# Performance work log

Measured on AMD Instinct MI355X. Metric: run time of the kernel, lower is better.

The kernel has to match this reference:

```python
import jax, jax.numpy as jnp
import numpy as np

B, T, H, NH = 2, 2048, 2048, 16
HD = H // NH
EPS = 1e-5

def gelu_tanh(x):
    c = jnp.sqrt(jnp.asarray(2.0 / jnp.pi, x.dtype))
    return 0.5 * x * (1.0 + jnp.tanh(c * (x + 0.044715 * x * x * x)))

def layer_norm(x, scale, shift):
    mean = jnp.mean(x, axis=-1, keepdims=True)
    var = jnp.mean((x - mean) ** 2, axis=-1, keepdims=True)  # unbiased=False
    return scale * ((x - mean) / jnp.sqrt(var + EPS)) + shift

def setup_inputs() -> dict:
    key = jax.random.key(0)
    ks = jax.random.split(key, 8)
    s = 0.02
    return {
        "x": jax.random.normal(ks[0], (B, T, H), dtype=jnp.float32),
        "wq": jax.random.normal(ks[1], (H, H), dtype=jnp.float32) * s,
        "wk": jax.random.normal(ks[2], (H, H), dtype=jnp.float32) * s,
        "wv": jax.random.normal(ks[3], (H, H), dtype=jnp.float32) * s,
        "wo": jax.random.normal(ks[4], (H, H), dtype=jnp.float32) * s,
        "ln1_scale": jnp.ones((H,), jnp.float32),
        "ln1_shift": jnp.zeros((H,), jnp.float32),
        "ln2_scale": jnp.ones((H,), jnp.float32),
        "ln2_shift": jnp.zeros((H,), jnp.float32),
        "w1": jax.random.normal(ks[5], (H, 4 * H), dtype=jnp.float32) * s,
        "b1": jnp.zeros((4 * H,), jnp.float32),
        "w2": jax.random.normal(ks[6], (4 * H, H), dtype=jnp.float32) * s,
        "b2": jnp.zeros((H,), jnp.float32),
    }

def reference(x, wq, wk, wv, wo, ln1_scale, ln1_shift, ln2_scale, ln2_shift, w1, b1, w2, b2):
    b, t, c = x.shape
    # --- attention sublayer (pre-norm, residual) ---
    h = layer_norm(x, ln1_scale, ln1_shift)
    q = (h @ wq).reshape(b, t, NH, HD).transpose(0, 2, 1, 3)  # [b,nh,t,hd]
    k = (h @ wk).reshape(b, t, NH, HD).transpose(0, 2, 1, 3)
    v = (h @ wv).reshape(b, t, NH, HD).transpose(0, 2, 1, 3)
    scores = jnp.einsum('bhqd,bhkd->bhqk', q, k) / jnp.sqrt(jnp.asarray(HD, jnp.float32))
    causal = jnp.triu(jnp.ones((t, t), jnp.bool_), k=1)
    scores = jnp.where(causal, -jnp.inf, scores)
    weights = jax.nn.softmax(scores, axis=-1)
    attn = jnp.einsum('bhqk,bhkd->bhqd', weights, v)
    attn = attn.transpose(0, 2, 1, 3).reshape(b, t, c)
    x = x + attn @ wo  # dropout is identity (drop_rate=0)
    # --- FFN sublayer ---
    h = layer_norm(x, ln2_scale, ln2_shift)
    h = gelu_tanh(h @ w1 + b1) @ w2 + b2
    return x + h
```

## Files before the change

### kernel.cpp

```cpp
#include <hip/hip_runtime.h>
#include <math.h>

#define HDIM 2048
#define NTOK 4096
#define NHEAD 16
#define HEADD 128
#define TSEQ 2048
#define NBATCH 2

typedef float f32x4 __attribute__((ext_vector_type(4)));
typedef short bf16x8 __attribute__((ext_vector_type(8)));

__device__ __forceinline__ unsigned short f2bf(float f) {
  union { float f; unsigned u; } v; v.f = f;
  unsigned r = v.u + 0x7FFFu + ((v.u >> 16) & 1u);
  return (unsigned short)(r >> 16);
}

__device__ __forceinline__ float gelu_tanh_f(float x) {
  float z = 0.7978845608028654f * (x + 0.044715f * x * x * x);
  float e = __expf(2.f * z);
  float th = 1.f - 2.f / (e + 1.f);
  return 0.5f * x * (1.f + th);
}

#define GLL16(g, l) __builtin_amdgcn_global_load_lds( \
    (const __attribute__((address_space(1))) unsigned int*)(g), \
    (__attribute__((address_space(3))) unsigned int*)(l), 16, 0, 0)

__global__ __launch_bounds__(256) void ln_kernel(const float* __restrict__ in,
                                                 const float* __restrict__ scale,
                                                 const float* __restrict__ shift,
                                                 unsigned short* __restrict__ out) {
  int row = blockIdx.x;
  int t = threadIdx.x;
  const float4* r4 = (const float4*)(in + (size_t)row * HDIM);
  float4 v0 = r4[t];
  float4 v1 = r4[t + 256];
  float sum = v0.x + v0.y + v0.z + v0.w + v1.x + v1.y + v1.z + v1.w;
  float sq  = v0.x*v0.x + v0.y*v0.y + v0.z*v0.z + v0.w*v0.w +
              v1.x*v1.x + v1.y*v1.y + v1.z*v1.z + v1.w*v1.w;
  for (int o = 32; o > 0; o >>= 1) {
    sum += __shfl_down(sum, o);
    sq  += __shfl_down(sq, o);
  }
  __shared__ float red[8];
  __shared__ float stat[2];
  int lane = t & 63, w = t >> 6;
  if (lane == 0) { red[w] = sum; red[4 + w] = sq; }
  __syncthreads();
  if (t == 0) {
    float s = red[0] + red[1] + red[2] + red[3];
    float q = red[4] + red[5] + red[6] + red[7];
    float mean = s / HDIM;
    float var = q / HDIM - mean * mean;
    stat[0] = mean;
    stat[1] = rsqrtf(var + 1e-5f);
  }
  __syncthreads();
  float mean = stat[0], rstd = stat[1];
  const float4* sc4 = (const float4*)scale;
  const float4* sh4 = (const float4*)shift;
  float4 s0 = sc4[t], s1 = sc4[t + 256];
  float4 h0 = sh4[t], h1 = sh4[t + 256];
  ushort4 a, b;
  a.x = f2bf(s0.x * ((v0.x - mean) * rstd) + h0.x);
  a.y = f2bf(s0.y * ((v0.y - mean) * rstd) + h0.y);
  a.z = f2bf(s0.z * ((v0.z - mean) * rstd) + h0.z);
  a.w = f2bf(s0.w * ((v0.w - mean) * rstd) + h0.w);
  b.x = f2bf(s1.x * ((v1.x - mean) * rstd) + h1.x);
  b.y = f2bf(s1.y * ((v1.y - mean) * rstd) + h1.y);
  b.z = f2bf(s1.z * ((v1.z - mean) * rstd) + h1.z);
  b.w = f2bf(s1.w * ((v1.w - mean) * rstd) + h1.w);
  *(ushort4*)&out[(size_t)row * HDIM + t * 4] = a;
  *(ushort4*)&out[(size_t)row * HDIM + 1024 + t * 4] = b;
}

__global__ __launch_bounds__(256) void castT_kernel(const float* __restrict__ W,
                                                    unsigned short* __restrict__ Wt,
                                                    int K, int N) {
  __shared__ float T[64][65];
  int k0 = blockIdx.x * 64, n0 = blockIdx.y * 64;
  int c = threadIdx.x & 15, r = threadIdx.x >> 4;
#pragma unroll
  for (int p = 0; p < 4; p++) {
    int kr = r + p * 16;
    float4 v = *(const float4*)&W[(size_t)(k0 + kr) * N + n0 + c * 4];
    T[kr][c * 4 + 0] = v.x; T[kr][c * 4 + 1] = v.y;
    T[kr][c * 4 + 2] = v.z; T[kr][c * 4 + 3] = v.w;
  }
  __syncthreads();
#pragma unroll
  for (int p = 0; p < 4; p++) {
    int nr = r + p * 16;
    ushort4 o;
    o.x = f2bf(T[c * 4 + 0][nr]);
    o.y = f2bf(T[c * 4 + 1][nr]);
    o.z = f2bf(T[c * 4 + 2][nr]);
    o.w = f2bf(T[c * 4 + 3][nr]);
    *(ushort4*)&Wt[(size_t)(n0 + nr) * K + k0 + c * 4] = o;
  }
}

__global__ __launch_bounds__(256) void gemm_bt(const unsigned short* __restrict__ A,
                                               const unsigned short* __restrict__ Bt,
                                               float* __restrict__ Cf,
                                               unsigned short* __restrict__ Cb,
                                               const float* __restrict__ bias,
                                               const float* __restrict__ resid,
                                               int M, int N, int K, int act_gelu,
                                               int qkv_mode,
                                               unsigned short* __restrict__ Qo,
                                               unsigned short* __restrict__ Ko,
                                               unsigned short* __restrict__ Vto,
                                               int rm, int rn, int xc) {
  __shared__ unsigned short ldsA[128 * 32];
  __shared__ unsigned short ldsB[128 * 32];
  int tid = threadIdx.x;
  int w = tid >> 6, lane = tid & 63;
  int lm = lane & 15, q = lane >> 4;
  int wm = w & 1, wn = w >> 1;

  int flat = blockIdx.y * gridDim.x + blockIdx.x;
  int xcd = flat & 7, l = flat >> 3;
  int tn_l = l % rn, tm_l = l / rn;
  int tm = (xcd / xc) * rm + tm_l;
  int tn = (xcd % xc) * rn + tn_l;
  int m0 = tm * 128, n0 = tn * 128;

  int row0, row1, kbg0, kbg1;
  {
    int o = w * 2048 + lane * 16;
    row0 = o >> 6; kbg0 = ((o >> 4) & 3) ^ ((row0 >> 1) & 3);
    o += 1024;
    row1 = o >> 6; kbg1 = ((o >> 4) & 3) ^ ((row1 >> 1) & 3);
  }
  const unsigned short* pa0 = A  + (size_t)(m0 + row0) * K + kbg0 * 8;
  const unsigned short* pa1 = A  + (size_t)(m0 + row1) * K + kbg1 * 8;
  const unsigned short* pb0 = Bt + (size_t)(n0 + row0) * K + kbg0 * 8;
  const unsigned short* pb1 = Bt + (size_t)(n0 + row1) * K + kbg1 * 8;
  unsigned short* la0 = ldsA + w * 1024;
  unsigned short* la1 = ldsA + w * 1024 + 512;
  unsigned short* lb0 = ldsB + w * 1024;
  unsigned short* lb1 = ldsB + w * 1024 + 512;

  f32x4 acc[4][4] = {};
  int s = (lm >> 1) & 3;
  int aoff[4], boff[4];
#pragma unroll
  for (int t = 0; t < 4; t++) {
    aoff[t] = ((wm * 64 + t * 16 + lm) << 5) + ((q ^ s) << 3);
    boff[t] = ((wn * 64 + t * 16 + lm) << 5) + ((q ^ s) << 3);
  }

  for (int k0 = 0; k0 < K; k0 += 32) {
    GLL16(pa0 + k0, la0);
    GLL16(pa1 + k0, la1);
    GLL16(pb0 + k0, lb0);
    GLL16(pb1 + k0, lb1);
    __syncthreads();
    bf16x8 af[4], bfv[4];
#pragma unroll
    for (int t = 0; t < 4; t++) af[t] = *(const bf16x8*)(ldsA + aoff[t]);
#pragma unroll
    for (int t = 0; t < 4; t++) bfv[t] = *(const bf16x8*)(ldsB + boff[t]);
#pragma unroll
    for (int mi = 0; mi < 4; mi++)
#pragma unroll
      for (int ni = 0; ni < 4; ni++)
        acc[mi][ni] = __builtin_amdgcn_mfma_f32_16x16x32_bf16(af[mi], bfv[ni], acc[mi][ni], 0, 0, 0);
    __syncthreads();
  }

  if (qkv_mode) {
#pragma unroll
    for (int ni = 0; ni < 4; ni++) {
      int n = n0 + wn * 64 + ni * 16 + lm;
      int region = n >> 11;
      int h = (n & 2047) >> 7, d = n & 127;
#pragma unroll
      for (int mi = 0; mi < 4; mi++) {
        int mb = m0 + wm * 64 + mi * 16 + q * 4;
        int b = mb >> 11, t0 = mb & 2047;
        if (region == 2) {
          ushort4 u;
          u.x = f2bf(acc[mi][ni][0]); u.y = f2bf(acc[mi][ni][1]);
          u.z = f2bf(acc[mi][ni][2]); u.w = f2bf(acc[mi][ni][3]);
          *(ushort4*)&Vto[(((size_t)(b * NHEAD + h)) * HEADD + d) * TSEQ + t0] = u;
        } else {
          unsigned short* dst = (region == 0) ? Qo : Ko;
          size_t base2 = (((size_t)(b * NHEAD + h)) * TSEQ + t0) * HEADD + d;
#pragma unroll
          for (int r = 0; r < 4; r++)
            dst[base2 + (size_t)r * HEADD] = f2bf(acc[mi][ni][r]);
        }
      }
    }
    return;
  }

#pragma unroll
  for (int ni = 0; ni < 4; ni++) {
    int n = n0 + wn * 64 + ni * 16 + lm;
    float bv = bias ? bias[n] : 0.f;
#pragma unroll
    for (int mi = 0; mi < 4; mi++) {
#pragma unroll
      for (int r = 0; r < 4; r++) {
        int m = m0 + wm * 64 + mi * 16 + q * 4 + r;
        float v = acc[mi][ni][r] + bv;
        if (act_gelu) v = gelu_tanh_f(v);
        if (resid) v += resid[(size_t)m * N + n];
        if (Cb) Cb[(size_t)m * N + n] = f2bf(v);
        else Cf[(size_t)m * N + n] = v;
      }
    }
  }
}

__global__ __launch_bounds__(256, 4) void attn_mfma(const unsigned short* __restrict__ Qb,
                                                    const unsigned short* __restrict__ Kb,
                                                    const unsigned short* __restrict__ Vtb,
                                                    unsigned short* __restrict__ O) {
  __shared__ unsigned short ldsK[64 * 128];
  __shared__ unsigned short ldsV[128 * 64];
  __shared__ unsigned short ldsP[64 * 64];

  int tid = threadIdx.x;
  int w = tid >> 6, lane = tid & 63;
  int lm = lane & 15, qd = lane >> 4;
  int qt = blockIdx.x, hh = blockIdx.y, bb = blockIdx.z;
  int q0 = qt * 64;
  size_t hbase = (size_t)(bb * NHEAD + hh) * (size_t)(TSEQ * HEADD);
  const unsigned short* Qh = Qb + hbase;
  const unsigned short* Kh = Kb + hbase;
  const unsigned short* Vh = Vtb + hbase;

  bf16x8 qf[4];
  {
    const unsigned short* qp = Qh + (size_t)(q0 + w * 16 + lm) * HEADD + qd * 8;
#pragma unroll
    for (int kc = 0; kc < 4; kc++) qf[kc] = *(const bf16x8*)(qp + kc * 32);
  }

  int koff[4], voff[4], ldst[4];
#pragma unroll
  for (int it = 0; it < 4; it++) {
    int ci = it * 256 + w * 64 + lane;
    int key = ci >> 4, pos = ci & 15;
    koff[it] = key * HEADD + ((pos ^ (key & 15)) << 3);
    int d = ci >> 3, pv = ci & 7;
    voff[it] = d * TSEQ + ((pv ^ (d & 7)) << 3);
    ldst[it] = (it * 256 + w * 64) * 8;
  }

  f32x4 oacc[8] = {};
  float mrow[4], lrow[4];
#pragma unroll
  for (int r = 0; r < 4; r++) { mrow[r] = -3.0e38f; lrow[r] = 0.f; }
  const float scl = 0.08838834764831845f;

  for (int kt = 0; kt <= qt; kt++) {
    int k0 = kt * 64;
    __syncthreads();
#pragma unroll
    for (int it = 0; it < 4; it++) {
      GLL16(Kh + (size_t)k0 * HEADD + koff[it], ldsK + ldst[it]);
      GLL16(Vh + k0 + voff[it], ldsV + ldst[it]);
    }
    __syncthreads();

    f32x4 sacc[4] = {};
#pragma unroll
    for (int kb = 0; kb < 4; kb++) {
#pragma unroll
      for (int kc = 0; kc < 4; kc++) {
        bf16x8 kf = *(const bf16x8*)(ldsK + (kb * 16 + lm) * HEADD + (((kc * 4 + qd) ^ lm) << 3));
        sacc[kb] = __builtin_amdgcn_mfma_f32_16x16x32_bf16(qf[kc], kf, sacc[kb], 0, 0, 0);
      }
    }

    float sv[4][4];
    int qrow_g = q0 + w * 16 + qd * 4;
    bool diag = (kt == qt);
#pragma unroll
    for (int kb = 0; kb < 4; kb++) {
      int key_g = k0 + kb * 16 + lm;
#pragma unroll
      for (int r = 0; r < 4; r++) {
        float x = sacc[kb][r] * scl;
        sv[kb][r] = (diag && key_g > qrow_g + r) ? -3.0e38f : x;
      }
    }
    float mloc[4];
#pragma unroll
    for (int r = 0; r < 4; r++)
      mloc[r] = fmaxf(fmaxf(sv[0][r], sv[1][r]), fmaxf(sv[2][r], sv[3][r]));
#pragma unroll
    for (int dm = 1; dm < 16; dm <<= 1)
#pragma unroll
      for (int r = 0; r < 4; r++) mloc[r] = fmaxf(mloc[r], __shfl_xor(mloc[r], dm));
    float al[4], lloc[4];
#pragma unroll
    for (int r = 0; r < 4; r++) {
      float mnew = fmaxf(mrow[r], mloc[r]);
      al[r] = __expf(mrow[r] - mnew);
      mrow[r] = mnew;
      lloc[r] = 0.f;
    }
#pragma unroll
    for (int kb = 0; kb < 4; kb++) {
#pragma unroll
      for (int r = 0; r < 4; r++) {
        float p = __expf(sv[kb][r] - mrow[r]);
        lloc[r] += p;
        int row = w * 16 + qd * 4 + r;
        int chunk = (kb * 2 + (lm >> 3)) ^ (row & 7);
        ldsP[row * 64 + chunk * 8 + (lm & 7)] = f2bf(p);
      }
    }
#pragma unroll
    for (int dm = 1; dm < 16; dm <<= 1)
#pragma unroll
      for (int r = 0; r < 4; r++) lloc[r] += __shfl_xor(lloc[r], dm);
#pragma unroll
    for (int r = 0; r < 4; r++) lrow[r] = lrow[r] * al[r] + lloc[r];
#pragma unroll
    for (int dt = 0; dt < 8; dt++)
#pragma unroll
      for (int r = 0; r < 4; r++) oacc[dt][r] *= al[r];

    bf16x8 pf[2];
#pragma unroll
    for (int kc2 = 0; kc2 < 2; kc2++)
      pf[kc2] = *(const bf16x8*)(ldsP + (w * 16 + lm) * 64 + (((kc2 * 4 + qd) ^ (lm & 7)) << 3));
#pragma unroll
    for (int dt = 0; dt < 8; dt++) {
#pragma unroll
      for (int kc2 = 0; kc2 < 2; kc2++) {
        bf16x8 vf = *(const bf16x8*)(ldsV + (dt * 16 + lm) * 64 + (((kc2 * 4 + qd) ^ (lm & 7)) << 3));
        oacc[dt] = __builtin_amdgcn_mfma_f32_16x16x32_bf16(pf[kc2], vf, oacc[dt], 0, 0, 0);
      }
    }
  }

  float inv[4];
#pragma unroll
  for (int r = 0; r < 4; r++) inv[r] = 1.f / lrow[r];
#pragma unroll
  for (int dt = 0; dt < 8; dt++) {
#pragma unroll
    for (int r = 0; r < 4; r++) {
      int t = q0 + w * 16 + qd * 4 + r;
      size_t idx = ((size_t)(bb * TSEQ + t)) * HDIM + hh * HEADD + dt * 16 + lm;
      O[idx] = f2bf(oacc[dt][r] * inv[r]);
    }
  }
}

extern "C" void kernel_launch(void* const* d_in, const int* in_sizes, int n_in,
                              void* d_out, int out_size, void* d_ws, size_t ws_size,
                              hipStream_t stream) {
  const float* x         = (const float*)d_in[0];
  const float* wq        = (const float*)d_in[1];
  const float* wk        = (const float*)d_in[2];
  const float* wv        = (const float*)d_in[3];
  const float* wo        = (const float*)d_in[4];
  const float* ln1_scale = (const float*)d_in[5];
  const float* ln1_shift = (const float*)d_in[6];
  const float* ln2_scale = (const float*)d_in[7];
  const float* ln2_shift = (const float*)d_in[8];
  const float* w1        = (const float*)d_in[9];
  const float* b1        = (const float*)d_in[10];
  const float* w2        = (const float*)d_in[11];
  const float* b2        = (const float*)d_in[12];

  char* ws = (char*)d_ws;
  const size_t MB = 1ull << 20;
  unsigned short* h1    = (unsigned short*)(ws);
  float*          x2    = (float*)(ws);
  unsigned short* Qb    = (unsigned short*)(ws + 32 * MB);
  unsigned short* Kb    = (unsigned short*)(ws + 48 * MB);
  unsigned short* Vtb   = (unsigned short*)(ws + 64 * MB);
  unsigned short* attnO = (unsigned short*)(ws + 80 * MB);
  unsigned short* woT   = (unsigned short*)(ws + 96 * MB);
  unsigned short* qkvT  = (unsigned short*)(ws + 104 * MB);
  unsigned short* a1    = (unsigned short*)(ws + 32 * MB);
  unsigned short* h2    = (unsigned short*)(ws + 96 * MB);
  unsigned short* w1T   = (unsigned short*)(ws + 128 * MB);
  unsigned short* w2T   = (unsigned short*)(ws + 160 * MB);

  dim3 blk(256);
  ln_kernel<<<NTOK, blk, 0, stream>>>(x, ln1_scale, ln1_shift, h1);
  castT_kernel<<<dim3(32, 32), blk, 0, stream>>>(wq, qkvT, 2048, 2048);
  castT_kernel<<<dim3(32, 32), blk, 0, stream>>>(wk, qkvT + (size_t)2048 * 2048, 2048, 2048);
  castT_kernel<<<dim3(32, 32), blk, 0, stream>>>(wv, qkvT + (size_t)4096 * 2048, 2048, 2048);
  castT_kernel<<<dim3(32, 32), blk, 0, stream>>>(wo, woT, 2048, 2048);
  castT_kernel<<<dim3(32, 128), blk, 0, stream>>>(w1, w1T, 2048, 8192);
  castT_kernel<<<dim3(128, 32), blk, 0, stream>>>(w2, w2T, 8192, 2048);
  gemm_bt<<<dim3(6144 / 128, 4096 / 128), blk, 0, stream>>>(
      h1, qkvT, nullptr, nullptr, nullptr, nullptr, 4096, 6144, 2048, 0, 1, Qb, Kb, Vtb,
      16, 12, 4);
  attn_mfma<<<dim3(TSEQ / 64, NHEAD, NBATCH), blk, 0, stream>>>(Qb, Kb, Vtb, attnO);
  gemm_bt<<<dim3(2048 / 128, 4096 / 128), blk, 0, stream>>>(
      attnO, woT, x2, nullptr, nullptr, x, 4096, 2048, 2048, 0, 0, nullptr, nullptr, nullptr,
      8, 8, 2);
  ln_kernel<<<NTOK, blk, 0, stream>>>(x2, ln2_scale, ln2_shift, h2);
  gemm_bt<<<dim3(8192 / 128, 4096 / 128), blk, 0, stream>>>(
      h2, w1T, nullptr, a1, b1, nullptr, 4096, 8192, 2048, 1, 0, nullptr, nullptr, nullptr,
      16, 16, 4);
  gemm_bt<<<dim3(2048 / 128, 4096 / 128), blk, 0, stream>>>(
      a1, w2T, (float*)d_out, nullptr, b2, x2, 4096, 2048, 8192, 0, 0, nullptr, nullptr, nullptr,
      8, 8, 2);
}
```

Measured before the change: 1.065 ms.

## Replace 128x128 GEMM with double-buffered 256-row, 8-wave pipelined MFMA GEMM

Replaces the simple single-buffered 128x128 bf16 GEMM with a templated 256xBN tile kernel using 512 threads, K-steps of 64, double-buffered LDS and a hand-scheduled sequence of four phases. Each phase interleaves global-to-LDS staging, LDS fragment loads and MFMA work, with explicit waitcnt, barriers and s_setprio. The goal is to overlap memory latency with compute and raise arithmetic intensity per tile, instead of stalling on a sync after every 32-wide K slice. The cost is larger LDS use and heavy register pressure from the 8xNIT accumulators. The fragile manual vmcnt and barrier choreography also adds correctness risk.

```diff
diff --git a/kernel.cpp b/kernel.cpp
--- a/kernel.cpp
+++ b/kernel.cpp
@@ -102,94 +102,194 @@
   }
 }
 
-__global__ __launch_bounds__(256) void gemm_bt(const unsigned short* __restrict__ A,
-                                               const unsigned short* __restrict__ Bt,
-                                               float* __restrict__ Cf,
-                                               unsigned short* __restrict__ Cb,
-                                               const float* __restrict__ bias,
-                                               const float* __restrict__ resid,
-                                               int M, int N, int K, int act_gelu,
-                                               int qkv_mode,
-                                               unsigned short* __restrict__ Qo,
-                                               unsigned short* __restrict__ Ko,
-                                               unsigned short* __restrict__ Vto,
-                                               int rm, int rn, int xc) {
-  __shared__ unsigned short ldsA[128 * 32];
-  __shared__ unsigned short ldsB[128 * 32];
-  int tid = threadIdx.x;
-  int w = tid >> 6, lane = tid & 63;
-  int lm = lane & 15, q = lane >> 4;
-  int wm = w & 1, wn = w >> 1;
+template<int BN>
+__global__ __launch_bounds__(512, 2) void gemm256(const unsigned short* __restrict__ A,
+                                                  const unsigned short* __restrict__ Bt,
+                                                  float* __restrict__ Cf,
+                                                  unsigned short* __restrict__ Cb,
+                                                  const float* __restrict__ bias,
+                                                  const float* __restrict__ resid,
+                                                  int M, int N, int K, int act_gelu,
+                                                  int qkv_mode,
+                                                  unsigned short* __restrict__ Qo,
+                                                  unsigned short* __restrict__ Ko,
+                                                  unsigned short* __restrict__ Vto,
+                                                  int rm, int rn, int xc) {
+  constexpr int NIT = BN / 64;
+  constexpr int NB  = NIT / 2;
+  constexpr int BSZ = BN * 64;
+
+  __shared__ unsigned short ldsA[2 * 16384];
+  __shared__ unsigned short ldsB[2 * BSZ];
+
+  const int tid = threadIdx.x;
+  const int w = tid >> 6, lane = tid & 63;
+  const int lm = lane & 15, qd = lane >> 4;
+  const int wm = w >> 2, wn = w & 3;
+  const int l8 = lane >> 3, l7 = lane & 7;
 
   int flat = blockIdx.y * gridDim.x + blockIdx.x;
   int xcd = flat & 7, l = flat >> 3;
   int tn_l = l % rn, tm_l = l / rn;
   int tm = (xcd / xc) * rm + tm_l;
   int tn = (xcd % xc) * rn + tn_l;
-  int m0 = tm * 128, n0 = tn * 128;
-
-  int row0, row1, kbg0, kbg1;
-  {
-    int o = w * 2048 + lane * 16;
-    row0 = o >> 6; kbg0 = ((o >> 4) & 3) ^ ((row0 >> 1) & 3);
-    o += 1024;
-    row1 = o >> 6; kbg1 = ((o >> 4) & 3) ^ ((row1 >> 1) & 3);
-  }
-  const unsigned short* pa0 = A  + (size_t)(m0 + row0) * K + kbg0 * 8;
-  const unsigned short* pa1 = A  + (size_t)(m0 + row1) * K + kbg1 * 8;
-  const unsigned short* pb0 = Bt + (size_t)(n0 + row0) * K + kbg0 * 8;
-  const unsigned short* pb1 = Bt + (size_t)(n0 + row1) * K + kbg1 * 8;
-  unsigned short* la0 = ldsA + w * 1024;
-  unsigned short* la1 = ldsA + w * 1024 + 512;
-  unsigned short* lb0 = ldsB + w * 1024;
-  unsigned short* lb1 = ldsB + w * 1024 + 512;
-
-  f32x4 acc[4][4] = {};
-  int s = (lm >> 1) & 3;
-  int aoff[4], boff[4];
-#pragma unroll
-  for (int t = 0; t < 4; t++) {
-    aoff[t] = ((wm * 64 + t * 16 + lm) << 5) + ((q ^ s) << 3);
-    boff[t] = ((wn * 64 + t * 16 + lm) << 5) + ((q ^ s) << 3);
-  }
-
-  for (int k0 = 0; k0 < K; k0 += 32) {
-    GLL16(pa0 + k0, la0);
-    GLL16(pa1 + k0, la1);
-    GLL16(pb0 + k0, lb0);
-    GLL16(pb1 + k0, lb1);
-    __syncthreads();
-    bf16x8 af[4], bfv[4];
-#pragma unroll
-    for (int t = 0; t < 4; t++) af[t] = *(const bf16x8*)(ldsA + aoff[t]);
-#pragma unroll
-    for (int t = 0; t < 4; t++) bfv[t] = *(const bf16x8*)(ldsB + boff[t]);
-#pragma unroll
-    for (int mi = 0; mi < 4; mi++)
-#pragma unroll
-      for (int ni = 0; ni < 4; ni++)
-        acc[mi][ni] = __builtin_amdgcn_mfma_f32_16x16x32_bf16(af[mi], bfv[ni], acc[mi][ni], 0, 0, 0);
-    __syncthreads();
-  }
+  int m0 = tm * 256, n0 = tn * BN;
+
+  const int swz = ((l7 ^ (l8 & 7)) << 3);
+  const int arb = wm * 128 + (w & 3) * 16;
+  const unsigned short* pAs = A + (size_t)(m0 + arb + l8) * K + swz;
+  unsigned short* lAs = ldsA + arb * 64;
+  const int brb = (BN == 256) ? ((w >> 1) * 64 + (w & 1) * 16)
+                              : ((w >> 1) * 32 + (w & 1) * 8);
+  const unsigned short* pBs = Bt + (size_t)(n0 + brb + l8) * K + swz;
+  unsigned short* lBs = ldsB + brb * 64;
+
+  const int ca0 = ((qd ^ l7) << 3);
+  const unsigned short* pAr = ldsA + (wm * 128 + lm) * 64;
+  const unsigned short* pBr = ldsB + (wn * (BN / 4) + lm) * 64;
+
+  f32x4 acc[8][NIT] = {};
+  bf16x8 a[2][4], b[2][NB];
+
+#define STAGE_A(buf, qm, kt) do { \
+    const unsigned short* _s = pAs + (size_t)(qm) * 64 * K + (size_t)(kt) * 64; \
+    unsigned short* _d = lAs + (buf) * 16384 + (qm) * 4096; \
+    GLL16(_s, _d); \
+    GLL16(_s + (size_t)8 * K, _d + 512); \
+  } while (0)
+
+#define STAGE_B(buf, qn, kt) do { \
+    if (BN == 256) { \
+      const unsigned short* _s = pBs + (size_t)(qn) * 32 * K + (size_t)(kt) * 64; \
+      unsigned short* _d = lBs + (buf) * BSZ + (qn) * 2048; \
+      GLL16(_s, _d); \
+      GLL16(_s + (size_t)8 * K, _d + 512); \
+    } else { \
+      const unsigned short* _s = pBs + (size_t)(qn) * 16 * K + (size_t)(kt) * 64; \
+      unsigned short* _d = lBs + (buf) * BSZ + (qn) * 1024; \
+      GLL16(_s, _d); \
+    } \
+  } while (0)
+
+#define LDA(buf, qm) do { \
+    _Pragma("unroll") \
+    for (int mi = 0; mi < 4; mi++) { \
+      a[0][mi] = *(const bf16x8*)(pAr + (buf) * 16384 + (qm) * 4096 + mi * 1024 + ca0); \
+      a[1][mi] = *(const bf16x8*)(pAr + (buf) * 16384 + (qm) * 4096 + mi * 1024 + (ca0 ^ 32)); \
+    } \
+  } while (0)
+
+#define LDB(buf, qn) do { \
+    _Pragma("unroll") \
+    for (int ni = 0; ni < NB; ni++) { \
+      b[0][ni] = *(const bf16x8*)(pBr + (buf) * BSZ + (qn) * (NB * 1024) + ni * 1024 + ca0); \
+      b[1][ni] = *(const bf16x8*)(pBr + (buf) * BSZ + (qn) * (NB * 1024) + ni * 1024 + (ca0 ^ 32)); \
+    } \
+  } while (0)
+
+#define MFMA_PH(qm, qn) do { \
+    __builtin_amdgcn_s_setprio(1); \
+    _Pragma("unroll") \
+    for (int ks = 0; ks < 2; ks++) \
+      _Pragma("unroll") \
+      for (int mi = 0; mi < 4; mi++) \
+        _Pragma("unroll") \
+        for (int ni = 0; ni < NB; ni++) \
+          acc[(qm) * 4 + mi][(qn) * NB + ni] = __builtin_amdgcn_mfma_f32_16x16x32_bf16( \
+              a[ks][mi], b[ks][ni], acc[(qm) * 4 + mi][(qn) * NB + ni], 0, 0, 0); \
+    __builtin_amdgcn_s_setprio(0); \
+  } while (0)
+
+#define BARX() do { asm volatile("" ::: "memory"); __builtin_amdgcn_s_barrier(); \
+                    asm volatile("" ::: "memory"); } while (0)
+#define LGKM0() do { asm volatile("s_waitcnt lgkmcnt(0)" ::: "memory"); \
+                     __builtin_amdgcn_sched_barrier(0); } while (0)
+#define VM_SS() do { if (BN == 256) asm volatile("s_waitcnt vmcnt(6)" ::: "memory"); \
+                     else           asm volatile("s_waitcnt vmcnt(5)" ::: "memory"); } while (0)
+#define VM_0()  do { asm volatile("s_waitcnt vmcnt(0)" ::: "memory"); } while (0)
+
+  const int niter = K >> 7;
+
+  STAGE_A(0, 0, 0); STAGE_B(0, 1, 0); STAGE_A(0, 1, 0); STAGE_B(0, 0, 0);
+  STAGE_A(1, 0, 1); STAGE_B(1, 1, 1); STAGE_A(1, 1, 1);
+  VM_SS();
+  BARX();
+
+  for (int i = 0; i < niter; ++i) {
+    const bool pf = (i + 1 < niter);
+    const int te = 2 * i + 2, to = 2 * i + 3;
+    LDA(0, 0); LDB(0, 0);
+    STAGE_B(1, 0, 2 * i + 1);
+    BARX(); LGKM0();
+    MFMA_PH(0, 0);
+    BARX();
+    LDB(0, 1);
+    if (pf) STAGE_A(0, 0, te);
+    BARX(); LGKM0();
+    MFMA_PH(0, 1);
+    BARX();
+    LDA(0, 1);
+    if (pf) STAGE_B(0, 1, te);
+    BARX(); LGKM0();
+    MFMA_PH(1, 1);
+    BARX();
+    LDB(0, 0);
+    if (pf) STAGE_A(0, 1, te);
+    BARX(); LGKM0();
+    MFMA_PH(1, 0);
+    if (pf) VM_SS(); else VM_0();
+    BARX();
+    LDA(1, 0); LDB(1, 0);
+    if (pf) STAGE_B(0, 0, te);
+    BARX(); LGKM0();
+    MFMA_PH(0, 0);
+    BARX();
+    LDB(1, 1);
+    if (pf) STAGE_A(1, 0, to);
+    BARX(); LGKM0();
+    MFMA_PH(0, 1);
+    BARX();
+    LDA(1, 1);
+    if (pf) STAGE_B(1, 1, to);
+    BARX(); LGKM0();
+    MFMA_PH(1, 1);
+    BARX();
+    LDB(1, 0);
+    if (pf) STAGE_A(1, 1, to);
+    BARX(); LGKM0();
+    MFMA_PH(1, 0);
+    if (pf) VM_SS();
+    BARX();
+  }
+
+#undef STAGE_A
+#undef STAGE_B
+#undef LDA
+#undef LDB
+#undef MFMA_PH
+#undef BARX
+#undef LGKM0
+#undef VM_SS
+#undef VM_0
 
   if (qkv_mode) {
 #pragma unroll
-    for (int ni = 0; ni < 4; ni++) {
-      int n = n0 + wn * 64 + ni * 16 + lm;
+    for (int ni = 0; ni < NIT; ni++) {
+      int n = n0 + wn * (BN / 4) + ni * 16 + lm;
       int region = n >> 11;
       int h = (n & 2047) >> 7, d = n & 127;
 #pragma unroll
-      for (int mi = 0; mi < 4; mi++) {
-        int mb = m0 + wm * 64 + mi * 16 + q * 4;
-        int b = mb >> 11, t0 = mb & 2047;
+      for (int mi = 0; mi < 8; mi++) {
+        int mb = m0 + wm * 128 + mi * 16 + qd * 4;
+        int bb = mb >> 11, t0 = mb & 2047;
         if (region == 2) {
           ushort4 u;
           u.x = f2bf(acc[mi][ni][0]); u.y = f2bf(acc[mi][ni][1]);
           u.z = f2bf(acc[mi][ni][2]); u.w = f2bf(acc[mi][ni][3]);
-          *(ushort4*)&Vto[(((size_t)(b * NHEAD + h)) * HEADD + d) * TSEQ + t0] = u;
+          *(ushort4*)&Vto[(((size_t)(bb * NHEAD + h)) * HEADD + d) * TSEQ + t0] = u;
         } else {
           unsigned short* dst = (region == 0) ? Qo : Ko;
-          size_t base2 = (((size_t)(b * NHEAD + h)) * TSEQ + t0) * HEADD + d;
+          size_t base2 = (((size_t)(bb * NHEAD + h)) * TSEQ + t0) * HEADD + d;
 #pragma unroll
           for (int r = 0; r < 4; r++)
             dst[base2 + (size_t)r * HEADD] = f2bf(acc[mi][ni][r]);
@@ -200,14 +300,14 @@
   }
 
 #pragma unroll
-  for (int ni = 0; ni < 4; ni++) {
-    int n = n0 + wn * 64 + ni * 16 + lm;
+  for (int ni = 0; ni < NIT; ni++) {
+    int n = n0 + wn * (BN / 4) + ni * 16 + lm;
     float bv = bias ? bias[n] : 0.f;
 #pragma unroll
-    for (int mi = 0; mi < 4; mi++) {
+    for (int mi = 0; mi < 8; mi++) {
 #pragma unroll
       for (int r = 0; r < 4; r++) {
-        int m = m0 + wm * 64 + mi * 16 + q * 4 + r;
+        int m = m0 + wm * 128 + mi * 16 + qd * 4 + r;
         float v = acc[mi][ni][r] + bv;
         if (act_gelu) v = gelu_tanh_f(v);
         if (resid) v += resid[(size_t)m * N + n];
@@ -390,7 +490,7 @@
   unsigned short* w1T   = (unsigned short*)(ws + 128 * MB);
   unsigned short* w2T   = (unsigned short*)(ws + 160 * MB);
 
-  dim3 blk(256);
+  dim3 blk(256), blk5(512);
   ln_kernel<<<NTOK, blk, 0, stream>>>(x, ln1_scale, ln1_shift, h1);
   castT_kernel<<<dim3(32, 32), blk, 0, stream>>>(wq, qkvT, 2048, 2048);
   castT_kernel<<<dim3(32, 32), blk, 0, stream>>>(wk, qkvT + (size_t)2048 * 2048, 2048, 2048);
@@ -398,18 +498,18 @@
   castT_kernel<<<dim3(32, 32), blk, 0, stream>>>(wo, woT, 2048, 2048);
   castT_kernel<<<dim3(32, 128), blk, 0, stream>>>(w1, w1T, 2048, 8192);
   castT_kernel<<<dim3(128, 32), blk, 0, stream>>>(w2, w2T, 8192, 2048);
-  gemm_bt<<<dim3(6144 / 128, 4096 / 128), blk, 0, stream>>>(
+  gemm256<128><<<dim3(48, 16), blk5, 0, stream>>>(
       h1, qkvT, nullptr, nullptr, nullptr, nullptr, 4096, 6144, 2048, 0, 1, Qb, Kb, Vtb,
-      16, 12, 4);
+      8, 12, 4);
   attn_mfma<<<dim3(TSEQ / 64, NHEAD, NBATCH), blk, 0, stream>>>(Qb, Kb, Vtb, attnO);
-  gemm_bt<<<dim3(2048 / 128, 4096 / 128), blk, 0, stream>>>(
+  gemm256<128><<<dim3(16, 16), blk5, 0, stream>>>(
       attnO, woT, x2, nullptr, nullptr, x, 4096, 2048, 2048, 0, 0, nullptr, nullptr, nullptr,
-      8, 8, 2);
+      4, 8, 2);
   ln_kernel<<<NTOK, blk, 0, stream>>>(x2, ln2_scale, ln2_shift, h2);
-  gemm_bt<<<dim3(8192 / 128, 4096 / 128), blk, 0, stream>>>(
+  gemm256<256><<<dim3(32, 16), blk5, 0, stream>>>(
       h2, w1T, nullptr, a1, b1, nullptr, 4096, 8192, 2048, 1, 0, nullptr, nullptr, nullptr,
-      16, 16, 4);
-  gemm_bt<<<dim3(2048 / 128, 4096 / 128), blk, 0, stream>>>(
+      8, 8, 4);
+  gemm256<128><<<dim3(16, 16), blk5, 0, stream>>>(
       a1, w2T, (float*)d_out, nullptr, b2, x2, 4096, 2048, 8192, 0, 0, nullptr, nullptr, nullptr,
-      8, 8, 2);
-}
+      4, 8, 2);
+}
```

Result: slower. 1.134 ms (+6.5%).
